# Kernel tuning notes

Measured on AMD Instinct MI355X. Metric: run time of the kernel, lower is better.

Reference implementation:

```python
import jax, jax.numpy as jnp
import numpy as np

B, S, D_IN, D_OUT, H = 2, 2048, 1024, 1024, 16
HD = D_OUT // H  # head dim = 64


def setup_inputs() -> dict:
    key = jax.random.key(0)
    ks = jax.random.split(key, 9)
    s_in = 1.0 / np.sqrt(D_IN)
    s_out = 1.0 / np.sqrt(D_OUT)
    return {
        "X": jax.random.normal(ks[0], (B, S, D_IN), dtype=jnp.float32),
        "Wq": jax.random.uniform(ks[1], (D_OUT, D_IN), jnp.float32, -s_in, s_in),
        "bq": jax.random.uniform(ks[2], (D_OUT,), jnp.float32, -s_in, s_in),
        "Wk": jax.random.uniform(ks[3], (D_OUT, D_IN), jnp.float32, -s_in, s_in),
        "bk": jax.random.uniform(ks[4], (D_OUT,), jnp.float32, -s_in, s_in),
        "Wv": jax.random.uniform(ks[5], (D_OUT, D_IN), jnp.float32, -s_in, s_in),
        "bv": jax.random.uniform(ks[6], (D_OUT,), jnp.float32, -s_in, s_in),
        "Wo": jax.random.uniform(ks[7], (D_OUT, D_OUT), jnp.float32, -s_out, s_out),
        "bo": jax.random.uniform(ks[8], (D_OUT,), jnp.float32, -s_out, s_out),
    }


def reference(X, Wq, bq, Wk, bk, Wv, bv, Wo, bo):
    scale = jnp.asarray(HD ** 0.5, X.dtype)  # self.dim = sqrt(head_dim)
    q = X @ Wq.T + bq  # [B,S,D_OUT]
    k = X @ Wk.T + bk
    v = X @ Wv.T + bv
    # split heads: b s (h d) -> b h s d
    q = q.reshape(B, S, H, HD).transpose(0, 2, 1, 3)
    k = k.reshape(B, S, H, HD).transpose(0, 2, 1, 3)
    v = v.reshape(B, S, H, HD).transpose(0, 2, 1, 3)
    scores = jnp.einsum('bhsd,bhtd->bhst', q, k) / scale  # [B,H,S,S]
    causal = jnp.triu(jnp.ones((S, S), dtype=bool), k=1)
    scores = jnp.where(causal, -jnp.inf, scores)
    weights = jax.nn.softmax(scores, axis=-1)
    out = jnp.einsum('bhst,bhtd->bhsd', weights, v)  # [B,H,S,HD]
    out = out.transpose(0, 2, 1, 3).reshape(B, S, D_OUT)  # b h s d -> b s (h d)
    return out @ Wo.T + bo
```

## Files before the change

kernel.cpp:

```cpp
#include <hip/hip_runtime.h>
#include <hip/hip_bf16.h>

typedef __bf16 bf16_t;
typedef __bf16 bf16x8 __attribute__((ext_vector_type(8)));
typedef float  f32x4  __attribute__((ext_vector_type(4)));
typedef unsigned short ushort_t;

#define MFMA16(a, b, c) __builtin_amdgcn_mfma_f32_16x16x32_bf16((a), (b), (c), 0, 0, 0)
#define GLDS16(g, l) __builtin_amdgcn_global_load_lds( \
    (const __attribute__((address_space(1))) unsigned int*)(g), \
    (__attribute__((address_space(3))) unsigned int*)(l), 16, 0, 0)

#define WAITCNT_VM(n)  (0x0F70 | (n))
#define WAITCNT_LGKM0  0xC07F

#define MEMFENCE asm volatile("" ::: "memory")

#define SWZ(r) ((((r) >> 1) ^ ((r) >> 3)) & 3)

#define QSCALE 0.18033688f

__global__ __launch_bounds__(256) void cvt_all(
    const void* __restrict__ X,  const void* __restrict__ W0, const void* __restrict__ W1,
    const void* __restrict__ W2, const void* __restrict__ W3,
    const void* __restrict__ c0, const void* __restrict__ c1,
    const void* __restrict__ c2, const void* __restrict__ c3,
    bf16_t* __restrict__ Xb, bf16_t* __restrict__ Wb, float* __restrict__ biasF,
    int* __restrict__ flag)
{
    const int tid  = threadIdx.x;
    const int lane = tid & 63;
    const ushort_t u = ((const ushort_t*)X)[2 * lane];
    const int e = (u >> 7) & 0xFF;
    const int f = (__ballot(e >= 0xA0) != 0ull) ? 1 : 0;

    const int bid = blockIdx.x;
    if (bid >= 4096) {
        if (bid == 4096 && tid == 0) *flag = f;
        const int idx = ((bid - 4096) * 256 + tid) * 8;
        const int w = idx >> 10, off = idx & 1023;
        const void* src = (w == 0) ? c0 : (w == 1) ? c1 : (w == 2) ? c2 : c3;
        #pragma unroll
        for (int r = 0; r < 8; ++r)
            biasF[idx + r] = f ? ((const float*)src)[off + r]
                               : (float)((const bf16_t*)src)[off + r];
        return;
    }

    const long long i = (long long)bid * 2048 + tid * 8;
    const void* src;
    bf16_t* dst;
    long long off;
    if (i < 4194304) { src = X; dst = Xb; off = i; }
    else {
        const int w = (int)((i - 4194304) >> 20);
        off = (i - 4194304) & 1048575;
        src = (w == 0) ? W0 : (w == 1) ? W1 : (w == 2) ? W2 : W3;
        dst = Wb + (size_t)w * 1048576;
    }
    if (f) {
        const float* s = (const float*)src + off;
        const float4 a = *(const float4*)(s);
        const float4 b = *(const float4*)(s + 4);
        bf16x8 o;
        o[0] = (bf16_t)a.x; o[1] = (bf16_t)a.y; o[2] = (bf16_t)a.z; o[3] = (bf16_t)a.w;
        o[4] = (bf16_t)b.x; o[5] = (bf16_t)b.y; o[6] = (bf16_t)b.z; o[7] = (bf16_t)b.w;
        *(bf16x8*)(dst + off) = o;
    } else {
        *(bf16x8*)(dst + off) = *(const bf16x8*)((const bf16_t*)src + off);
    }
}

template<int TM>
__global__ __launch_bounds__(256, 3) void gemm_nt(
    const bf16_t* __restrict__ A,
    const bf16_t* __restrict__ W0, const bf16_t* __restrict__ W1, const bf16_t* __restrict__ W2,
    const float* __restrict__ b0, const float* __restrict__ b1, const float* __restrict__ b2,
    void* __restrict__ C, int ldc, bf16_t* __restrict__ Vt, int fuse_vt,
    const int* __restrict__ flag, int is_out)
{
    constexpr int MI = TM / 32;
    __shared__ bf16_t Ash[2][TM * 32];
    __shared__ bf16_t Bsh[2][128 * 32];

    const int f32out = is_out ? *flag : 0;

    const int tid  = threadIdx.x;
    const int wid  = tid >> 6;
    const int lane = tid & 63;
    const int g    = lane >> 4;
    const int c    = lane & 15;

    int bx = blockIdx.x, by = blockIdx.y;
    if (fuse_vt) {
        const int flat = by * 32 + bx;
        const int xcd = flat & 7, lid = flat >> 3;
        const int xg = xcd & 3, yg = xcd >> 2;
        bx = xg * 8 + (lid & 7);
        by = yg * 12 + (lid >> 3);
    }

    const int m0  = bx * TM;
    const int n0  = by * 128;
    const int mat = n0 >> 10;
    const bf16_t* W  = (mat == 0) ? W0 : (mat == 1) ? W1 : W2;
    const float*  bs = (mat == 0) ? b0 : (mat == 1) ? b1 : b2;
    const int nw = n0 & 1023;

    const int srow = lane >> 2;
    const int sblk = (lane & 3) ^ ((lane >> 3) & 3);
    const bf16_t* Ag = A + (size_t)(m0 + wid * (TM / 4) + srow) * 1024 + sblk * 8;
    const bf16_t* Wg = W + (size_t)(nw + wid * 32 + srow) * 1024 + sblk * 8;

    const int waveM = (wid >> 1) * (TM / 2);
    const int waveN = (wid & 1) * 64;

    f32x4 acc[MI][4] = {};
    const int fblk = (g ^ ((c >> 1) & 3)) * 8;

    auto stage = [&](int t) {
        const int k0 = t * 32;
        const int buf = t & 1;
        bf16_t* As = &Ash[buf][(wid * (TM / 4)) * 32];
        bf16_t* Bs = &Bsh[buf][(wid * 32) * 32];
        GLDS16(Ag + k0, As);
        if (TM == 128) GLDS16(Ag + (size_t)16 * 1024 + k0, As + 16 * 32);
        GLDS16(Wg + k0, Bs);
        GLDS16(Wg + (size_t)16 * 1024 + k0, Bs + 16 * 32);
    };

    stage(0);
    __builtin_amdgcn_s_waitcnt(WAITCNT_VM(0));
    __builtin_amdgcn_s_barrier();
    MEMFENCE;

    #pragma unroll 2
    for (int k = 0; k < 32; ++k) {
        const int cur = k & 1;
        bf16x8 af[MI], bfr[4];
        #pragma unroll
        for (int i = 0; i < MI; ++i)
            af[i] = *(const bf16x8*)(&Ash[cur][(waveM + i * 16 + c) * 32 + fblk]);
        #pragma unroll
        for (int j = 0; j < 4; ++j)
            bfr[j] = *(const bf16x8*)(&Bsh[cur][(waveN + j * 16 + c) * 32 + fblk]);

        if (k < 31) stage(k + 1);

        __builtin_amdgcn_s_setprio(1);
        #pragma unroll
        for (int i = 0; i < MI; ++i)
            #pragma unroll
            for (int j = 0; j < 4; ++j)
                acc[i][j] = MFMA16(af[i], bfr[j], acc[i][j]);
        __builtin_amdgcn_s_setprio(0);

        MEMFENCE;
        __builtin_amdgcn_s_waitcnt(WAITCNT_LGKM0);
        if (k < 31) __builtin_amdgcn_s_waitcnt(WAITCNT_VM(0));
        __builtin_amdgcn_s_barrier();
        MEMFENCE;
    }

    if (fuse_vt && mat == 2) {
        #pragma unroll
        for (int j = 0; j < 4; ++j) {
            const int col  = n0 + waveN + j * 16 + c;
            const int hcol = col & 1023;
            const float bv = bs[hcol];
            const int h = hcol >> 6, d = hcol & 63;
            #pragma unroll
            for (int i = 0; i < MI; ++i) {
                const int row = m0 + waveM + i * 16 + g * 4;
                const int bb = row >> 11, s = row & 2047;
                bf16_t pk[4];
                #pragma unroll
                for (int r = 0; r < 4; ++r) pk[r] = (bf16_t)(acc[i][j][r] + bv);
                *(uint2*)(&Vt[(((size_t)bb * 16 + h) * 64 + d) * 2048 + s]) = *(uint2*)pk;
            }
        }
        return;
    }

    const float oscale = (fuse_vt && mat == 0) ? QSCALE : 1.0f;
    #pragma unroll
    for (int j = 0; j < 4; ++j) {
        const int col = n0 + waveN + j * 16 + c;
        const float bv = bs[col & 1023];
        #pragma unroll
        for (int i = 0; i < MI; ++i) {
            const int row = m0 + waveM + i * 16 + g * 4;
            #pragma unroll
            for (int r = 0; r < 4; ++r) {
                const float val = (acc[i][j][r] + bv) * oscale;
                const size_t idx = (size_t)(row + r) * ldc + col;
                if (f32out) ((float*)C)[idx] = val;
                else        ((bf16_t*)C)[idx] = (bf16_t)val;
            }
        }
    }
}

__global__ __launch_bounds__(256, 4) void attn_kernel(
    const bf16_t* __restrict__ QKV, const bf16_t* __restrict__ Vt,
    bf16_t* __restrict__ O)
{
    __shared__ bf16_t Ksh[2][64][32];
    __shared__ bf16_t Vsh[2][64][32];
    __shared__ bf16_t Psh[4][2][16][32];

    const int tid  = threadIdx.x;
    const int wid  = tid >> 6;
    const int lane = tid & 63;
    const int g    = lane >> 4;
    const int c    = lane & 15;

    const int bh = blockIdx.y;
    const int b  = bh >> 4, h = bh & 15;
    const int qt = (bh < 16) ? blockIdx.x : (31 - blockIdx.x);
    const int q0 = qt * 64;
    const int nt = qt + 1;

    bf16x8 aq[2];
    {
        const bf16_t* qp = QKV + (size_t)(b * 2048 + q0 + wid * 16 + c) * 3072 + h * 64;
        aq[0] = *(const bf16x8*)(qp + g * 8);
        aq[1] = *(const bf16x8*)(qp + 32 + g * 8);
    }

    float li[4] = {};
    f32x4 o[4]  = {};

    const int sr = tid >> 2;
    const int j4 = tid & 3;
    const bf16_t* Kg = QKV + (size_t)(b * 2048 + sr) * 3072 + 1024 + h * 64 + j4 * 16;
    const bf16_t* Vg = Vt + ((size_t)bh * 64 + sr) * 2048 + j4 * 16;

    const int ssr = SWZ(sr);
    const int bb0 = j4 * 2, bb1 = bb0 + 1;
    bf16_t* kd0 = &Ksh[bb0 >> 2][sr][((bb0 & 3) ^ ssr) * 8];
    bf16_t* kd1 = &Ksh[bb1 >> 2][sr][((bb1 & 3) ^ ssr) * 8];
    bf16_t* vd0 = &Vsh[bb0 >> 2][sr][((bb0 & 3) ^ ssr) * 8];
    bf16_t* vd1 = &Vsh[bb1 >> 2][sr][((bb1 & 3) ^ ssr) * 8];

    uint4 kr0 = *(const uint4*)(Kg);
    uint4 kr1 = *(const uint4*)(Kg + 8);
    uint4 vr0 = *(const uint4*)(Vg);
    uint4 vr1 = *(const uint4*)(Vg + 8);

    for (int jt = 0; jt < nt; ++jt) {
        *(uint4*)kd0 = kr0;
        *(uint4*)kd1 = kr1;
        *(uint4*)vd0 = vr0;
        *(uint4*)vd1 = vr1;
        __syncthreads();

        if (jt + 1 < nt) {
            const size_t ko = (size_t)(jt + 1) * 64 * 3072;
            kr0 = *(const uint4*)(Kg + ko);
            kr1 = *(const uint4*)(Kg + ko + 8);
            vr0 = *(const uint4*)(Vg + (jt + 1) * 64);
            vr1 = *(const uint4*)(Vg + (jt + 1) * 64 + 8);
        }

        f32x4 s[4] = {};
        __builtin_amdgcn_s_setprio(1);
        #pragma unroll
        for (int n = 0; n < 4; ++n)
            #pragma unroll
            for (int kb = 0; kb < 2; ++kb) {
                const int row = n * 16 + c;
                const bf16x8 kf = *(const bf16x8*)(&Ksh[kb][row][(g ^ SWZ(row)) * 8]);
                s[n] = MFMA16(aq[kb], kf, s[n]);
            }
        __builtin_amdgcn_s_setprio(0);

        if (jt == nt - 1) {
            const int j0 = jt * 64;
            const int qrow = q0 + wid * 16 + g * 4;
            #pragma unroll
            for (int n = 0; n < 4; ++n)
                #pragma unroll
                for (int r = 0; r < 4; ++r)
                    if (j0 + n * 16 + c > qrow + r) s[n][r] = -1e30f;
        }

        #pragma unroll
        for (int n = 0; n < 4; ++n)
            #pragma unroll
            for (int r = 0; r < 4; ++r) {
                const float p = __builtin_amdgcn_exp2f(s[n][r]);
                li[r] += p;
                const int q  = g * 4 + r;
                const int gg = 2 * n + (c >> 3);
                Psh[wid][gg >> 2][q][((gg & 3) ^ SWZ(q)) * 8 + (c & 7)] = (bf16_t)p;
            }
        __builtin_amdgcn_wave_barrier();

        __builtin_amdgcn_s_setprio(1);
        #pragma unroll
        for (int kb = 0; kb < 2; ++kb) {
            const bf16x8 ap = *(const bf16x8*)(&Psh[wid][kb][c][(g ^ SWZ(c)) * 8]);
            #pragma unroll
            for (int d = 0; d < 4; ++d) {
                const int row = d * 16 + c;
                const bf16x8 vf = *(const bf16x8*)(&Vsh[kb][row][(g ^ SWZ(row)) * 8]);
                o[d] = MFMA16(ap, vf, o[d]);
            }
        }
        __builtin_amdgcn_s_setprio(0);
        __syncthreads();
    }

    #pragma unroll
    for (int off = 1; off < 16; off <<= 1)
        #pragma unroll
        for (int r = 0; r < 4; ++r)
            li[r] += __shfl_xor(li[r], off, 64);

    const int orow = b * 2048 + q0 + wid * 16 + g * 4;
    #pragma unroll
    for (int r = 0; r < 4; ++r) {
        const float inv = 1.0f / li[r];
        #pragma unroll
        for (int d = 0; d < 4; ++d)
            O[(size_t)(orow + r) * 1024 + h * 64 + d * 16 + c] = (bf16_t)(o[d][r] * inv);
    }
}

extern "C" void kernel_launch(void* const* d_in, const int* in_sizes, int n_in,
                              void* d_out, int out_size, void* d_ws, size_t ws_size,
                              hipStream_t stream)
{
    const void* X  = d_in[0];
    const void* Wq = d_in[1];  const void* bq = d_in[2];
    const void* Wk = d_in[3];  const void* bk = d_in[4];
    const void* Wv = d_in[5];  const void* bv = d_in[6];
    const void* Wo = d_in[7];  const void* bo = d_in[8];

    int*    flag  = (int*)d_ws;
    float*  biasF = (float*)((char*)d_ws + 16);
    bf16_t* Xb    = (bf16_t*)((char*)d_ws + 16 + 16384);
    bf16_t* Wb    = Xb  + (size_t)4096 * 1024;
    bf16_t* QKV   = Wb  + (size_t)4 * 1024 * 1024;
    bf16_t* Vt    = QKV + (size_t)4096 * 3072;
    bf16_t* Ao    = Vt  + (size_t)4096 * 1024;

    const size_t MW = (size_t)1024 * 1024;

    cvt_all<<<4098, 256, 0, stream>>>(X, Wq, Wk, Wv, Wo, bq, bk, bv, bo,
                                      Xb, Wb, biasF, flag);

    gemm_nt<128><<<dim3(32, 24), 256, 0, stream>>>(
        Xb, Wb, Wb + MW, Wb + 2 * MW,
        biasF, biasF + 1024, biasF + 2048, QKV, 3072, Vt, 1, flag, 0);
    attn_kernel<<<dim3(32, 32), 256, 0, stream>>>(QKV, Vt, Ao);
    gemm_nt<64><<<dim3(64, 8), 256, 0, stream>>>(
        Ao, Wb + 3 * MW, Wb + 3 * MW, Wb + 3 * MW,
        biasF + 3072, biasF + 3072, biasF + 3072, d_out, 1024, (bf16_t*)nullptr, 0, flag, 1);
}
```

Baseline: 205.0 us.

## Add 256x256-tile QKV GEMM kernel with 4-stage LDS pipeline

Replaces the 128x128-tile QKV projection GEMM with a dedicated 512-thread kernel that computes 256x256 output tiles, so each wave handles a 128x64 sub-tile. It uses a 4-buffer LDS ring with loads issued three k-steps ahead to hide global latency. The larger tile increases operand reuse per byte loaded. The grid shrinks to 192 blocks, fewer than the CU count, and per-block LDS rises to 128KB, which may leave CUs idle and cut occupancy. The XCD block-remapping is dropped, and the old generic GEMM is reduced to serve only the output projection.

```diff
diff --git a/kernel.cpp b/kernel.cpp
--- a/kernel.cpp
+++ b/kernel.cpp
@@ -71,12 +71,127 @@
     }
 }
 
+__global__ __launch_bounds__(512, 2) void gemm256(
+    const bf16_t* __restrict__ A,
+    const bf16_t* __restrict__ W0, const bf16_t* __restrict__ W1, const bf16_t* __restrict__ W2,
+    const float* __restrict__ b0, const float* __restrict__ b1, const float* __restrict__ b2,
+    bf16_t* __restrict__ C, bf16_t* __restrict__ Vt)
+{
+    __shared__ bf16_t Ash[4][256 * 32];
+    __shared__ bf16_t Bsh[4][256 * 32];
+
+    const int tid  = threadIdx.x;
+    const int wid  = tid >> 6;
+    const int lane = tid & 63;
+    const int g    = lane >> 4;
+    const int c    = lane & 15;
+
+    const int m0  = blockIdx.x * 256;
+    const int n0  = blockIdx.y * 256;
+    const int mat = n0 >> 10;
+    const bf16_t* W  = (mat == 0) ? W0 : (mat == 1) ? W1 : W2;
+    const float*  bs = (mat == 0) ? b0 : (mat == 1) ? b1 : b2;
+    const int nw = n0 & 1023;
+
+    const int srow = lane >> 2;
+    const int sblk = (lane & 3) ^ ((lane >> 3) & 3);
+    const bf16_t* Ag = A + (size_t)(m0 + wid * 32 + srow) * 1024 + sblk * 8;
+    const bf16_t* Wg = W + (size_t)(nw + wid * 32 + srow) * 1024 + sblk * 8;
+
+    const int waveM = (wid >> 2) * 128;
+    const int waveN = (wid & 3) * 64;
+    const int fblk  = (g ^ ((c >> 1) & 3)) * 8;
+
+    f32x4 acc[8][4] = {};
+
+    auto stageA = [&](int H, int q) {
+        GLDS16(Ag + (size_t)(q * 16) * 1024 + H * 32, &Ash[H & 3][(wid * 32 + q * 16) * 32]);
+    };
+    auto stageB = [&](int H, int q) {
+        GLDS16(Wg + (size_t)(q * 16) * 1024 + H * 32, &Bsh[H & 3][(wid * 32 + q * 16) * 32]);
+    };
+
+    for (int H = 0; H < 3; ++H) {
+        stageA(H, 0); stageA(H, 1); stageB(H, 0); stageB(H, 1);
+    }
+    __builtin_amdgcn_s_waitcnt(WAITCNT_VM(8));
+    __builtin_amdgcn_s_barrier();
+    MEMFENCE;
+
+    #pragma unroll 4
+    for (int H = 0; H < 32; ++H) {
+        const int buf = H & 3;
+        const bf16_t* As = Ash[buf];
+        const bf16_t* Bs = Bsh[buf];
+
+        bf16x8 bfr[4], af[8];
+        #pragma unroll
+        for (int j = 0; j < 4; ++j)
+            bfr[j] = *(const bf16x8*)(&Bs[(waveN + j * 16 + c) * 32 + fblk]);
+        #pragma unroll
+        for (int i = 0; i < 8; ++i)
+            af[i] = *(const bf16x8*)(&As[(waveM + i * 16 + c) * 32 + fblk]);
+
+        if (H < 29) { stageA(H + 3, 0); stageA(H + 3, 1); stageB(H + 3, 0); stageB(H + 3, 1); }
+
+        __builtin_amdgcn_s_setprio(1);
+        #pragma unroll
+        for (int i = 0; i < 8; ++i)
+            #pragma unroll
+            for (int j = 0; j < 4; ++j)
+                acc[i][j] = MFMA16(af[i], bfr[j], acc[i][j]);
+        __builtin_amdgcn_s_setprio(0);
+
+        MEMFENCE;
+        __builtin_amdgcn_s_waitcnt(WAITCNT_LGKM0);
+        if (H < 29)       __builtin_amdgcn_s_waitcnt(WAITCNT_VM(8));
+        else if (H == 29) __builtin_amdgcn_s_waitcnt(WAITCNT_VM(4));
+        else if (H == 30) __builtin_amdgcn_s_waitcnt(WAITCNT_VM(0));
+        __builtin_amdgcn_s_barrier();
+        MEMFENCE;
+    }
+
+    if (mat == 2) {
+        #pragma unroll
+        for (int j = 0; j < 4; ++j) {
+            const int col  = n0 + waveN + j * 16 + c;
+            const int hcol = col & 1023;
+            const float bv = bs[hcol];
+            const int h = hcol >> 6, d = hcol & 63;
+            #pragma unroll
+            for (int i = 0; i < 8; ++i) {
+                const int row = m0 + waveM + i * 16 + g * 4;
+                const int bb = row >> 11, s = row & 2047;
+                bf16_t pk[4];
+                #pragma unroll
+                for (int r = 0; r < 4; ++r) pk[r] = (bf16_t)(acc[i][j][r] + bv);
+                *(uint2*)(&Vt[(((size_t)bb * 16 + h) * 64 + d) * 2048 + s]) = *(uint2*)pk;
+            }
+        }
+        return;
+    }
+
+    const float os = (mat == 0) ? QSCALE : 1.0f;
+    #pragma unroll
+    for (int j = 0; j < 4; ++j) {
+        const int col = n0 + waveN + j * 16 + c;
+        const float bv = bs[col & 1023];
+        #pragma unroll
+        for (int i = 0; i < 8; ++i) {
+            const int row = m0 + waveM + i * 16 + g * 4;
+            #pragma unroll
+            for (int r = 0; r < 4; ++r)
+                C[(size_t)(row + r) * 3072 + col] = (bf16_t)((acc[i][j][r] + bv) * os);
+        }
+    }
+}
+
 template<int TM>
 __global__ __launch_bounds__(256, 3) void gemm_nt(
     const bf16_t* __restrict__ A,
-    const bf16_t* __restrict__ W0, const bf16_t* __restrict__ W1, const bf16_t* __restrict__ W2,
-    const float* __restrict__ b0, const float* __restrict__ b1, const float* __restrict__ b2,
-    void* __restrict__ C, int ldc, bf16_t* __restrict__ Vt, int fuse_vt,
+    const bf16_t* __restrict__ W0,
+    const float* __restrict__ b0,
+    void* __restrict__ C, int ldc,
     const int* __restrict__ flag, int is_out)
 {
     constexpr int MI = TM / 32;
@@ -91,20 +206,10 @@
     const int g    = lane >> 4;
     const int c    = lane & 15;
 
-    int bx = blockIdx.x, by = blockIdx.y;
-    if (fuse_vt) {
-        const int flat = by * 32 + bx;
-        const int xcd = flat & 7, lid = flat >> 3;
-        const int xg = xcd & 3, yg = xcd >> 2;
-        bx = xg * 8 + (lid & 7);
-        by = yg * 12 + (lid >> 3);
-    }
-
-    const int m0  = bx * TM;
-    const int n0  = by * 128;
-    const int mat = n0 >> 10;
-    const bf16_t* W  = (mat == 0) ? W0 : (mat == 1) ? W1 : W2;
-    const float*  bs = (mat == 0) ? b0 : (mat == 1) ? b1 : b2;
+    const int m0  = blockIdx.x * TM;
+    const int n0  = blockIdx.y * 128;
+    const bf16_t* W  = W0;
+    const float*  bs = b0;
     const int nw = n0 & 1023;
 
     const int srow = lane >> 2;
@@ -162,27 +267,6 @@
         MEMFENCE;
     }
 
-    if (fuse_vt && mat == 2) {
-        #pragma unroll
-        for (int j = 0; j < 4; ++j) {
-            const int col  = n0 + waveN + j * 16 + c;
-            const int hcol = col & 1023;
-            const float bv = bs[hcol];
-            const int h = hcol >> 6, d = hcol & 63;
-            #pragma unroll
-            for (int i = 0; i < MI; ++i) {
-                const int row = m0 + waveM + i * 16 + g * 4;
-                const int bb = row >> 11, s = row & 2047;
-                bf16_t pk[4];
-                #pragma unroll
-                for (int r = 0; r < 4; ++r) pk[r] = (bf16_t)(acc[i][j][r] + bv);
-                *(uint2*)(&Vt[(((size_t)bb * 16 + h) * 64 + d) * 2048 + s]) = *(uint2*)pk;
-            }
-        }
-        return;
-    }
-
-    const float oscale = (fuse_vt && mat == 0) ? QSCALE : 1.0f;
     #pragma unroll
     for (int j = 0; j < 4; ++j) {
         const int col = n0 + waveN + j * 16 + c;
@@ -192,7 +276,7 @@
             const int row = m0 + waveM + i * 16 + g * 4;
             #pragma unroll
             for (int r = 0; r < 4; ++r) {
-                const float val = (acc[i][j][r] + bv) * oscale;
+                const float val = acc[i][j][r] + bv;
                 const size_t idx = (size_t)(row + r) * ldc + col;
                 if (f32out) ((float*)C)[idx] = val;
                 else        ((bf16_t*)C)[idx] = (bf16_t)val;
@@ -351,11 +435,10 @@
     cvt_all<<<4098, 256, 0, stream>>>(X, Wq, Wk, Wv, Wo, bq, bk, bv, bo,
                                       Xb, Wb, biasF, flag);
 
-    gemm_nt<128><<<dim3(32, 24), 256, 0, stream>>>(
+    gemm256<<<dim3(16, 12), 512, 0, stream>>>(
         Xb, Wb, Wb + MW, Wb + 2 * MW,
-        biasF, biasF + 1024, biasF + 2048, QKV, 3072, Vt, 1, flag, 0);
+        biasF, biasF + 1024, biasF + 2048, QKV, Vt);
     attn_kernel<<<dim3(32, 32), 256, 0, stream>>>(QKV, Vt, Ao);
     gemm_nt<64><<<dim3(64, 8), 256, 0, stream>>>(
-        Ao, Wb + 3 * MW, Wb + 3 * MW, Wb + 3 * MW,
-        biasF + 3072, biasF + 3072, biasF + 3072, d_out, 1024, (bf16_t*)nullptr, 0, flag, 1);
+        Ao, Wb + 3 * MW, biasF + 3072, d_out, 1024, flag, 1);
 }
```

New measurement: 202.1 us. About the same (-1.4%).
